# Kernel optimization log

Measured on AMD Instinct MI355X. Metric: run time of the kernel, lower is better.

Reference implementation:

```python
import jax, jax.numpy as jnp
import numpy as np

NUM_TERMS = 8
NUM_CHANNELS = 64
BATCH = 8
NODES = 2048


def setup_inputs() -> dict:
    key = jax.random.key(0)
    kA, kh = jax.random.split(key)
    A = jax.random.normal(kA, (BATCH, NODES, NODES), dtype=jnp.float32)
    # xavier_uniform over (num_terms+1, num_channels)
    fan_in, fan_out = NUM_TERMS + 1, NUM_CHANNELS
    limit = float(np.sqrt(6.0 / (fan_in + fan_out)))
    h = jax.random.uniform(kh, (NUM_TERMS + 1, NUM_CHANNELS), dtype=jnp.float32,
                           minval=-limit, maxval=limit)
    return {"A": A, "h": h}


def reference(A, h):
    # Y[b,n,c] = h[0,c] + sum_{i=1..T} h[i,c] * diag(A^i)[b,n]
    num_terms = h.shape[0] - 1
    diags = []  # each [B, N]: diagonal of A^i
    Ap = A
    for i in range(num_terms):
        if i > 0:
            Ap = jnp.matmul(Ap, A)  # A^(i+1), computed once per power
        diags.append(jnp.diagonal(Ap, axis1=-2, axis2=-1))
    D = jnp.stack(diags, axis=0)  # [T, B, N]
    # fuse per-channel weighted sum of diagonals into one einsum
    out = jnp.einsum("tbn,tc->bnc", D, h[1:])
    out = out + h[0][None, None, :]  # identity term: diag(I) == 1
    return out
```

## Files before the change

kernel.cpp:

```cpp
#include <hip/hip_runtime.h>
#include <hip/hip_bf16.h>

#define NN 2048
#define BB 8
#define NC 64
#define NTILE 32
#define NITER 16

typedef __bf16 bf16_8 __attribute__((ext_vector_type(8)));
typedef __bf16 bf16_4 __attribute__((ext_vector_type(4)));
typedef float f32x16 __attribute__((ext_vector_type(16)));

__device__ __forceinline__ void gll16(const void* g, void* l) {
  __builtin_amdgcn_global_load_lds((const __attribute__((address_space(1))) void*)g,
                                   (__attribute__((address_space(3))) void*)l,
                                   16, 0, 0);
}

__global__ __launch_bounds__(256)
void k_convert(const float* __restrict__ A, __bf16* __restrict__ Ab, __bf16* __restrict__ At) {
  __shared__ __bf16 tile[64][65];
  int b = blockIdx.z;
  const float* Asrc = A + (size_t)b * NN * NN;
  __bf16* Abd = Ab + (size_t)b * NN * NN;
  __bf16* Atd = At + (size_t)b * NN * NN;
  int r0 = blockIdx.y * 64, c0 = blockIdx.x * 64;
  int row = threadIdx.x >> 4;
  int col4 = (threadIdx.x & 15) * 4;
#pragma unroll
  for (int rr = 0; rr < 64; rr += 16) {
    float4 v = *(const float4*)&Asrc[(size_t)(r0 + row + rr) * NN + c0 + col4];
    bf16_4 hv;
    hv[0] = (__bf16)v.x; hv[1] = (__bf16)v.y; hv[2] = (__bf16)v.z; hv[3] = (__bf16)v.w;
    *(bf16_4*)&Abd[(size_t)(r0 + row + rr) * NN + c0 + col4] = hv;
    tile[row + rr][col4 + 0] = hv[0];
    tile[row + rr][col4 + 1] = hv[1];
    tile[row + rr][col4 + 2] = hv[2];
    tile[row + rr][col4 + 3] = hv[3];
  }
  __syncthreads();
  int row2 = threadIdx.x >> 3;
  int col8 = (threadIdx.x & 7) * 8;
#pragma unroll
  for (int rr = 0; rr < 64; rr += 32) {
    bf16_8 v;
#pragma unroll
    for (int j = 0; j < 8; ++j) v[j] = tile[col8 + j][row2 + rr];
    *(bf16_8*)&Atd[(size_t)(c0 + row2 + rr) * NN + r0 + col8] = v;
  }
}

__device__ __forceinline__
void gemm_body256(const __bf16* __restrict__ Pb, const __bf16* __restrict__ Qb,
                  __bf16* __restrict__ Cb, __bf16* __restrict__ Ctb,
                  __bf16* smem, int tmBlk, int tnBlk) {
  __bf16 (*As)[256][64] = (__bf16(*)[256][64])smem;
  __bf16 (*Bs)[256][64] = (__bf16(*)[256][64])(smem + 32768);
  const int tid = threadIdx.x;
  const int wave = tid >> 6, lane = tid & 63;
  const int wm = wave >> 2, wn = wave & 3;
  const int tm = tmBlk * 256, tn = tnBlk * 256;
  const int am = lane & 31, ah = lane >> 5;
  const int rx = (am >> 1) & 7;

  const int sr = lane >> 3;
  const int sc = (lane & 7) ^ (((wave & 1) * 4 + (lane >> 4)) & 7);
  const __bf16* srcA = Pb + (size_t)(tm + wave * 8 + sr) * NN + sc * 8;
  const __bf16* srcB = Qb + (size_t)(tn + wave * 8 + sr) * NN + sc * 8;

#define STAGE(Tc_, s_, bufT_)                                                  \
  do {                                                                         \
    if ((s_) == 0) {                                                 \
      const __bf16* s0 = srcA + (size_t)(Tc_) * 64;                            \
      gll16(s0,                   &As[bufT_][wave * 8][0]);                    \
      gll16(s0 + (size_t)64 * NN, &As[bufT_][64 + wave * 8][0]);               \
    } else if ((s_) == 1) {                                          \
      const __bf16* s0 = srcB + (size_t)128 * NN + (size_t)(Tc_) * 64;         \
      gll16(s0,                   &Bs[bufT_][128 + wave * 8][0]);              \
      gll16(s0 + (size_t)64 * NN, &Bs[bufT_][192 + wave * 8][0]);              \
    } else if ((s_) == 2) {                                          \
      const __bf16* s0 = srcA + (size_t)128 * NN + (size_t)(Tc_) * 64;         \
      gll16(s0,                   &As[bufT_][128 + wave * 8][0]);              \
      gll16(s0 + (size_t)64 * NN, &As[bufT_][192 + wave * 8][0]);              \
    } else {                                                         \
      const __bf16* s0 = srcB + (size_t)(Tc_) * 64;                            \
      gll16(s0,                   &Bs[bufT_][wave * 8][0]);                    \
      gll16(s0 + (size_t)64 * NN, &Bs[bufT_][64 + wave * 8][0]);               \
    }                                                                          \
  } while (0)

  STAGE(0, 0, 0); STAGE(0, 3, 0); STAGE(0, 2, 0); STAGE(0, 1, 0);
  STAGE(1, 0, 1); STAGE(1, 3, 1); STAGE(1, 2, 1); STAGE(1, 1, 1);
  asm volatile("s_waitcnt vmcnt(8)" ::: "memory");
  __builtin_amdgcn_s_barrier();

  f32x16 acc[4][2] = {};
  bf16_8 af[2][4], bfr[2][4];

  {
    const int rb0 = wn * 32 + am;
#pragma unroll
    for (int ks = 0; ks < 4; ++ks)
      bfr[0][ks] = *(const bf16_8*)&Bs[0][rb0][((2 * ks + ah) ^ rx) * 8];
  }

  for (int it = 0; it < NITER; ++it) {
#pragma unroll
    for (int p = 0; p < 8; ++p) {
      const int q = p & 3;
      const int rbuf = p >> 2;
      const int i0 = (q >> 1) * 2;
      const int in = (q == 1 || q == 2) ? 1 : 0;
      if (q == 0) {
#pragma unroll
        for (int i = 0; i < 2; ++i) {
          const int ra = (2 * i + wm) * 32 + am;
#pragma unroll
          for (int ks = 0; ks < 4; ++ks)
            af[i][ks] = *(const bf16_8*)&As[rbuf][ra][((2 * ks + ah) ^ rx) * 8];
        }
      } else if (q == 1) {
        const int rb1 = (4 + wn) * 32 + am;
#pragma unroll
        for (int ks = 0; ks < 4; ++ks)
          bfr[1][ks] = *(const bf16_8*)&Bs[rbuf][rb1][((2 * ks + ah) ^ rx) * 8];
      } else if (q == 2) {
#pragma unroll
        for (int i = 0; i < 2; ++i) {
          const int ra = (4 + 2 * i + wm) * 32 + am;
#pragma unroll
          for (int ks = 0; ks < 4; ++ks)
            af[i][ks] = *(const bf16_8*)&As[rbuf][ra][((2 * ks + ah) ^ rx) * 8];
        }
      }
      if (p == 1) {
        int T = 2 * it + 2; if (T > NTILE - 1) T = NTILE - 1;
        STAGE(T, 0, 0); STAGE(T, 3, 0);
      } else if (p == 2) {
        int T = 2 * it + 2; if (T > NTILE - 1) T = NTILE - 1;
        STAGE(T, 1, 0);
      } else if (p == 3) {
        int T = 2 * it + 2; if (T > NTILE - 1) T = NTILE - 1;
        STAGE(T, 2, 0);
      } else if (p == 5) {
        int T = 2 * it + 3; if (T > NTILE - 1) T = NTILE - 1;
        STAGE(T, 0, 1); STAGE(T, 3, 1);
      } else if (p == 6) {
        int T = 2 * it + 3; if (T > NTILE - 1) T = NTILE - 1;
        STAGE(T, 1, 1);
      } else if (p == 7) {
        int T = 2 * it + 3; if (T > NTILE - 1) T = NTILE - 1;
        STAGE(T, 2, 1);
      }

      if (q == 3) asm volatile("s_waitcnt vmcnt(8)" ::: "memory");
      __builtin_amdgcn_s_barrier();
      if (q != 3) asm volatile("s_waitcnt lgkmcnt(0)" ::: "memory");
      __builtin_amdgcn_s_setprio(1);
#pragma unroll
      for (int ks = 0; ks < 4; ++ks)
#pragma unroll
        for (int i = 0; i < 2; ++i)
          acc[i0 + i][in] = __builtin_amdgcn_mfma_f32_32x32x16_bf16(
              af[i][ks], bfr[in][ks], acc[i0 + i][in], 0, 0, 0);
      __builtin_amdgcn_s_setprio(0);
      if (q == 3) {
        const int rb0 = wn * 32 + am;
#pragma unroll
        for (int ks = 0; ks < 4; ++ks)
          bfr[0][ks] = *(const bf16_8*)&Bs[rbuf ^ 1][rb0][((2 * ks + ah) ^ rx) * 8];
      }
      __builtin_amdgcn_s_barrier();
    }
  }
  asm volatile("s_waitcnt vmcnt(0) lgkmcnt(0)" ::: "memory");

  const int cc = am;
  const int rq = ah * 4;
#pragma unroll
  for (int im = 0; im < 4; ++im)
#pragma unroll
    for (int in = 0; in < 2; ++in)
#pragma unroll
      for (int reg = 0; reg < 16; ++reg) {
        int row = (reg & 3) + 8 * (reg >> 2) + rq;
        Cb[(size_t)(tm + (2 * im + wm) * 32 + row) * NN +
           (tn + (4 * in + wn) * 32 + cc)] = (__bf16)acc[im][in][reg];
      }

  if (Ctb != nullptr) {
    __syncthreads();
    __bf16 (*Tt)[264] = (__bf16(*)[264])smem;
#pragma unroll
    for (int ch = 0; ch < 4; ++ch) {
      if ((wn >> 1) == (ch & 1)) {
        const int inw = ch >> 1;
#pragma unroll
        for (int im = 0; im < 4; ++im)
#pragma unroll
          for (int g = 0; g < 4; ++g) {
            bf16_4 v;
#pragma unroll
            for (int r = 0; r < 4; ++r) v[r] = (__bf16)acc[im][inw][g * 4 + r];
            *(bf16_4*)&Tt[(wn & 1) * 32 + cc][(2 * im + wm) * 32 + 8 * g + rq] = v;
          }
      }
      __syncthreads();
#pragma unroll
      for (int rr = 0; rr < 4; ++rr) {
        int trow = rr * 16 + (tid >> 5);
        int tcol = (tid & 31) * 8;
        bf16_8 v = *(const bf16_8*)&Tt[trow][tcol];
        *(bf16_8*)&Ctb[(size_t)(tn + ch * 64 + trow) * NN + tm + tcol] = v;
      }
      __syncthreads();
    }
  }
#undef STAGE
}

__global__ __launch_bounds__(512, 2)
void k_gemm1(const __bf16* __restrict__ Ab, const __bf16* __restrict__ At,
             __bf16* __restrict__ A2, __bf16* __restrict__ A2t) {
  __shared__ __align__(16) __bf16 smem[65536];
  size_t mb = (size_t)blockIdx.z * NN * NN;
  gemm_body256(Ab + mb, At + mb, A2 + mb, A2t + mb, smem, blockIdx.y, blockIdx.x);
}

__global__ __launch_bounds__(512, 2)
void k_gemm23(const __bf16* __restrict__ At, const __bf16* __restrict__ A2,
              const __bf16* __restrict__ A2t,
              __bf16* __restrict__ A3t, __bf16* __restrict__ A4,
              __bf16* __restrict__ A4t) {
  __shared__ __align__(16) __bf16 smem[65536];
  int job = blockIdx.z >> 3;
  size_t mb = (size_t)(blockIdx.z & 7) * NN * NN;
  if (job == 0)
    gemm_body256(At + mb, A2 + mb, A3t + mb, nullptr, smem, blockIdx.y, blockIdx.x);
  else
    gemm_body256(A2 + mb, A2t + mb, A4 + mb, A4t + mb, smem, blockIdx.y, blockIdx.x);
}

__global__ __launch_bounds__(256)
void k_reduce(const float* __restrict__ A, const float* __restrict__ h,
              const __bf16* __restrict__ A2, const __bf16* __restrict__ A3t,
              const __bf16* __restrict__ A4, const __bf16* __restrict__ A4t,
              float* __restrict__ out) {
  int b = blockIdx.y;
  int wave = threadIdx.x >> 6, lane = threadIdx.x & 63;
  int n = blockIdx.x * 4 + wave;
  size_t mb = (size_t)b * NN * NN;
  size_t rb = mb + (size_t)n * NN;
  float d5 = 0, d6 = 0, d7 = 0, d8 = 0;
  for (int c = 0; c < NN; c += 512) {
    int k = c + lane * 8;
    bf16_8 va2  = *(const bf16_8*)(A2 + rb + k);
    bf16_8 va3t = *(const bf16_8*)(A3t + rb + k);
    bf16_8 va4  = *(const bf16_8*)(A4 + rb + k);
    bf16_8 va4t = *(const bf16_8*)(A4t + rb + k);
#pragma unroll
    for (int j = 0; j < 8; ++j) {
      float f2 = (float)va2[j], f4 = (float)va4[j];
      float f3t = (float)va3t[j], f4t = (float)va4t[j];
      d5 += f2 * f3t;
      d6 += f2 * f4t;
      d7 += f4 * f3t;
      d8 += f4 * f4t;
    }
  }
#pragma unroll
  for (int off = 32; off > 0; off >>= 1) {
    d5 += __shfl_xor(d5, off);
    d6 += __shfl_xor(d6, off);
    d7 += __shfl_xor(d7, off);
    d8 += __shfl_xor(d8, off);
  }
  float d1 = A[mb + (size_t)n * NN + n];
  float d2 = (float)A2[rb + n];
  float d3 = (float)A3t[rb + n];
  float d4 = (float)A4[rb + n];
  float r = h[lane] + h[64 + lane] * d1 + h[128 + lane] * d2 + h[192 + lane] * d3 +
            h[256 + lane] * d4 + h[320 + lane] * d5 + h[384 + lane] * d6 +
            h[448 + lane] * d7 + h[512 + lane] * d8;
  out[((size_t)b * NN + n) * NC + lane] = r;
}

extern "C" void kernel_launch(void* const* d_in, const int* in_sizes, int n_in,
                              void* d_out, int out_size, void* d_ws, size_t ws_size,
                              hipStream_t stream) {
  const float* A = (const float*)d_in[0];
  const float* h = (const float*)d_in[1];
  float* out = (float*)d_out;

  size_t elems = (size_t)BB * NN * NN;
  __bf16* Ab  = (__bf16*)d_ws;
  __bf16* At  = Ab + elems;
  __bf16* A2  = At + elems;
  __bf16* A2t = A2 + elems;
  __bf16* A3t = A2t + elems;
  __bf16* A4  = A3t + elems;
  __bf16* A4t = Ab;

  k_convert<<<dim3(32, 32, BB), dim3(256), 0, stream>>>(A, Ab, At);
  k_gemm1<<<dim3(8, 8, BB), dim3(512), 0, stream>>>(Ab, At, A2, A2t);
  k_gemm23<<<dim3(8, 8, 2 * BB), dim3(512), 0, stream>>>(At, A2, A2t, A3t, A4, A4t);
  k_reduce<<<dim3(NN / 4, BB), dim3(256), 0, stream>>>(A, h, A2, A3t, A4, A4t, out);
}
```

Measured before the change: 663.1 us.

## Restructure GEMM main loop into two half-phases with reordered staged prefetch

Replaces the 8-phase-per-iteration pipeline with two phases per buffer. Each phase loads A and B fragments, issues 16 MFMAs, then reloads the other A fragments and issues 16 more. Global-to-LDS staging is regrouped so one quarter of the next tile is prefetched early into the other buffer and the rest after the mid-barrier, with vmcnt(6) waits. This cuts the barrier count and makes each MFMA burst longer. In exchange it holds more fragments live in registers and is more exposed to synchronisation hazards if the wait counts or buffer indexing are wrong.

New measurement: 660.9 us. Within noise of the previous version (-0.3%).

```diff
diff --git a/kernel.cpp b/kernel.cpp
--- a/kernel.cpp
+++ b/kernel.cpp
@@ -89,87 +89,81 @@
     }                                                                          \
   } while (0)
 
-  STAGE(0, 0, 0); STAGE(0, 3, 0); STAGE(0, 2, 0); STAGE(0, 1, 0);
-  STAGE(1, 0, 1); STAGE(1, 3, 1); STAGE(1, 2, 1); STAGE(1, 1, 1);
-  asm volatile("s_waitcnt vmcnt(8)" ::: "memory");
+  STAGE(0, 0, 0); STAGE(0, 3, 0); STAGE(0, 1, 0); STAGE(0, 2, 0);
+  STAGE(1, 0, 1); STAGE(1, 3, 1); STAGE(1, 1, 1);
+  asm volatile("s_waitcnt vmcnt(6)" ::: "memory");
   __builtin_amdgcn_s_barrier();
 
   f32x16 acc[4][2] = {};
   bf16_8 af[2][4], bfr[2][4];
 
-  {
-    const int rb0 = wn * 32 + am;
-#pragma unroll
-    for (int ks = 0; ks < 4; ++ks)
-      bfr[0][ks] = *(const bf16_8*)&Bs[0][rb0][((2 * ks + ah) ^ rx) * 8];
-  }
-
   for (int it = 0; it < NITER; ++it) {
 #pragma unroll
-    for (int p = 0; p < 8; ++p) {
-      const int q = p & 3;
-      const int rbuf = p >> 2;
-      const int i0 = (q >> 1) * 2;
-      const int in = (q == 1 || q == 2) ? 1 : 0;
-      if (q == 0) {
+    for (int h = 0; h < 2; ++h) {
+      const int b = h;
+#pragma unroll
+      for (int ks = 0; ks < 4; ++ks) {
+        const int ra = (0 * 2 + wm) * 32 + am;
+        af[0][ks] = *(const bf16_8*)&As[b][ra][((2 * ks + ah) ^ rx) * 8];
+      }
+#pragma unroll
+      for (int ks = 0; ks < 4; ++ks) {
+        const int rb0 = wn * 32 + am;
+        bfr[0][ks] = *(const bf16_8*)&Bs[b][rb0][((2 * ks + ah) ^ rx) * 8];
+      }
+#pragma unroll
+      for (int ks = 0; ks < 4; ++ks) {
+        const int ra = (1 * 2 + wm) * 32 + am;
+        af[1][ks] = *(const bf16_8*)&As[b][ra][((2 * ks + ah) ^ rx) * 8];
+      }
+#pragma unroll
+      for (int ks = 0; ks < 4; ++ks) {
+        const int rb1 = (4 + wn) * 32 + am;
+        bfr[1][ks] = *(const bf16_8*)&Bs[b][rb1][((2 * ks + ah) ^ rx) * 8];
+      }
+      {
+        int T = 2 * it + h + 1; if (T > NTILE - 1) T = NTILE - 1;
+        STAGE(T, 2, b ^ 1);
+      }
+      __builtin_amdgcn_s_setprio(1);
+#pragma unroll
+      for (int ks = 0; ks < 4; ++ks) {
 #pragma unroll
         for (int i = 0; i < 2; ++i) {
-          const int ra = (2 * i + wm) * 32 + am;
-#pragma unroll
-          for (int ks = 0; ks < 4; ++ks)
-            af[i][ks] = *(const bf16_8*)&As[rbuf][ra][((2 * ks + ah) ^ rx) * 8];
+          acc[i][0] = __builtin_amdgcn_mfma_f32_32x32x16_bf16(
+              af[i][ks], bfr[0][ks], acc[i][0], 0, 0, 0);
+          acc[i][1] = __builtin_amdgcn_mfma_f32_32x32x16_bf16(
+              af[i][ks], bfr[1][ks], acc[i][1], 0, 0, 0);
         }
-      } else if (q == 1) {
-        const int rb1 = (4 + wn) * 32 + am;
+      }
+      __builtin_amdgcn_s_setprio(0);
+      __builtin_amdgcn_sched_barrier(0);
+      __builtin_amdgcn_s_barrier();
+#pragma unroll
+      for (int i = 0; i < 2; ++i) {
+        const int ra = (4 + 2 * i + wm) * 32 + am;
 #pragma unroll
         for (int ks = 0; ks < 4; ++ks)
-          bfr[1][ks] = *(const bf16_8*)&Bs[rbuf][rb1][((2 * ks + ah) ^ rx) * 8];
-      } else if (q == 2) {
+          af[i][ks] = *(const bf16_8*)&As[b][ra][((2 * ks + ah) ^ rx) * 8];
+      }
+      {
+        int T = 2 * it + h + 2; if (T > NTILE - 1) T = NTILE - 1;
+        STAGE(T, 0, b); STAGE(T, 3, b); STAGE(T, 1, b);
+      }
+      __builtin_amdgcn_s_setprio(1);
+#pragma unroll
+      for (int ks = 0; ks < 4; ++ks) {
 #pragma unroll
         for (int i = 0; i < 2; ++i) {
-          const int ra = (4 + 2 * i + wm) * 32 + am;
-#pragma unroll
-          for (int ks = 0; ks < 4; ++ks)
-            af[i][ks] = *(const bf16_8*)&As[rbuf][ra][((2 * ks + ah) ^ rx) * 8];
+          acc[2 + i][1] = __builtin_amdgcn_mfma_f32_32x32x16_bf16(
+              af[i][ks], bfr[1][ks], acc[2 + i][1], 0, 0, 0);
+          acc[2 + i][0] = __builtin_amdgcn_mfma_f32_32x32x16_bf16(
+              af[i][ks], bfr[0][ks], acc[2 + i][0], 0, 0, 0);
         }
       }
-      if (p == 1) {
-        int T = 2 * it + 2; if (T > NTILE - 1) T = NTILE - 1;
-        STAGE(T, 0, 0); STAGE(T, 3, 0);
-      } else if (p == 2) {
-        int T = 2 * it + 2; if (T > NTILE - 1) T = NTILE - 1;
-        STAGE(T, 1, 0);
-      } else if (p == 3) {
-        int T = 2 * it + 2; if (T > NTILE - 1) T = NTILE - 1;
-        STAGE(T, 2, 0);
-      } else if (p == 5) {
-        int T = 2 * it + 3; if (T > NTILE - 1) T = NTILE - 1;
-        STAGE(T, 0, 1); STAGE(T, 3, 1);
-      } else if (p == 6) {
-        int T = 2 * it + 3; if (T > NTILE - 1) T = NTILE - 1;
-        STAGE(T, 1, 1);
-      } else if (p == 7) {
-        int T = 2 * it + 3; if (T > NTILE - 1) T = NTILE - 1;
-        STAGE(T, 2, 1);
-      }
-
-      if (q == 3) asm volatile("s_waitcnt vmcnt(8)" ::: "memory");
-      __builtin_amdgcn_s_barrier();
-      if (q != 3) asm volatile("s_waitcnt lgkmcnt(0)" ::: "memory");
-      __builtin_amdgcn_s_setprio(1);
-#pragma unroll
-      for (int ks = 0; ks < 4; ++ks)
-#pragma unroll
-        for (int i = 0; i < 2; ++i)
-          acc[i0 + i][in] = __builtin_amdgcn_mfma_f32_32x32x16_bf16(
-              af[i][ks], bfr[in][ks], acc[i0 + i][in], 0, 0, 0);
       __builtin_amdgcn_s_setprio(0);
-      if (q == 3) {
-        const int rb0 = wn * 32 + am;
-#pragma unroll
-        for (int ks = 0; ks < 4; ++ks)
-          bfr[0][ks] = *(const bf16_8*)&Bs[rbuf ^ 1][rb0][((2 * ks + ah) ^ rx) * 8];
-      }
+      asm volatile("s_waitcnt vmcnt(6)" ::: "memory");
+      __builtin_amdgcn_sched_barrier(0);
       __builtin_amdgcn_s_barrier();
     }
   }
```
